# Optimization experiments

Measured on AMD Instinct MI355X. Metric: run time of the kernel, lower is better.

## Reference

```python
import jax, jax.numpy as jnp
import numpy as np

N_HEADS = 16
D_MODEL = 1024
D_K = D_MODEL // N_HEADS
B, T = 2, 2048


def setup_inputs() -> dict:
    key = jax.random.key(0)
    ks = jax.random.split(key, 12)
    s = 1.0 / np.sqrt(D_MODEL)
    inp = {
        "q": jax.random.normal(ks[0], (B, T, D_MODEL), jnp.float32),
        "k": jax.random.normal(ks[1], (B, T, D_MODEL), jnp.float32),
        "v": jax.random.normal(ks[2], (B, T, D_MODEL), jnp.float32),
        # weights stored as [in, out] (torch Linear weight transposed)
        "Wq": jax.random.normal(ks[3], (D_MODEL, D_MODEL), jnp.float32) * s,
        "bq": jax.random.normal(ks[4], (D_MODEL,), jnp.float32) * s,
        "Wk": jax.random.normal(ks[5], (D_MODEL, D_MODEL), jnp.float32) * s,
        "bk": jax.random.normal(ks[6], (D_MODEL,), jnp.float32) * s,
        "Wv": jax.random.normal(ks[7], (D_MODEL, D_MODEL), jnp.float32) * s,
        "bv": jax.random.normal(ks[8], (D_MODEL,), jnp.float32) * s,
        "Wo": jax.random.normal(ks[9], (D_MODEL, D_MODEL), jnp.float32) * s,
        "bo": jax.random.normal(ks[10], (D_MODEL,), jnp.float32) * s,
        "alpha": jnp.ones((1, N_HEADS, 1, 1), jnp.float32) * 10.0,
    }
    return inp


def reference(q, k, v, Wq, bq, Wk, bk, Wv, bv, Wo, bo, alpha):
    Bsz, Tlen, _ = q.shape

    def proj(x, W, b):
        # [B,T,D] -> [B,H,T,d_k]
        y = x @ W + b
        return y.reshape(Bsz, Tlen, N_HEADS, D_K).transpose(0, 2, 1, 3)

    qh = proj(q, Wq, bq)
    kh = proj(k, Wk, bk)
    vh = proj(v, Wv, bv)

    scores = jnp.einsum("bhqd,bhkd->bhqk", qh, kh)  # [B,H,T,T]
    norm_q = jnp.linalg.norm(qh, axis=-1)  # [B,H,T]
    norm_k = jnp.linalg.norm(kh, axis=-1)  # [B,H,T]
    D_udps = (norm_q[..., :, None] + norm_k[..., None, :]) ** 2  # [B,H,T,T]
    D_safe = jnp.where(D_udps == 0.0, jnp.inf, D_udps)
    scores = alpha * 4.0 * scores / D_safe
    attn = jax.nn.softmax(scores, axis=-1)
    out = jnp.einsum("bhqk,bhkd->bhqd", attn, vh)
    out = out.transpose(0, 2, 1, 3).reshape(Bsz, Tlen, D_MODEL)
    return out @ Wo + bo
```

## Files before the change

kernel.cpp:

```cpp
#include <hip/hip_runtime.h>
#include <hip/hip_bf16.h>

#define N_HEADS 16
#define D_MODEL 1024
#define D_K     64
#define B_SZ    2
#define T_LEN   2048
#define M_ROWS  (B_SZ * T_LEN)

typedef __bf16 bf16;
typedef __bf16 bf16x4 __attribute__((ext_vector_type(4)));
typedef __bf16 bf16x8 __attribute__((ext_vector_type(8)));
typedef float  f32x4  __attribute__((ext_vector_type(4)));
typedef unsigned int u32;

__device__ __forceinline__ void gload16(const bf16* g, bf16* l) {
    __builtin_amdgcn_global_load_lds(
        (const __attribute__((address_space(1))) u32*)g,
        (__attribute__((address_space(3))) u32*)l, 16, 0, 0);
}

#define WAIT_VM(N) asm volatile("s_waitcnt vmcnt(" #N ")" ::: "memory")

__global__ void wt_kernel(const float* __restrict__ W0, const float* __restrict__ W1,
                          const float* __restrict__ W2, const float* __restrict__ W3,
                          bf16* __restrict__ T0, bf16* __restrict__ T1,
                          bf16* __restrict__ T2, bf16* __restrict__ T3) {
    __shared__ float tile[32][33];
    const int z = blockIdx.z;
    const float* W = (z == 0) ? W0 : (z == 1) ? W1 : (z == 2) ? W2 : W3;
    bf16* Wt       = (z == 0) ? T0 : (z == 1) ? T1 : (z == 2) ? T2 : T3;
    const int tx = threadIdx.x, ty = threadIdx.y;
    const int x0 = blockIdx.x * 32, y0 = blockIdx.y * 32;
    for (int yy = ty; yy < 32; yy += 8)
        tile[yy][tx] = W[(size_t)(y0 + yy) * D_MODEL + x0 + tx];
    __syncthreads();
    for (int yy = ty; yy < 32; yy += 8)
        Wt[(size_t)(x0 + yy) * D_MODEL + y0 + tx] = (bf16)tile[tx][yy];
}

__global__ void conv3_kernel(const float* __restrict__ q, const float* __restrict__ k,
                             const float* __restrict__ v,
                             bf16* __restrict__ qb, bf16* __restrict__ kb,
                             bf16* __restrict__ vb) {
    const int z = blockIdx.y;
    const float* X = (z == 0) ? q : (z == 1) ? k : v;
    bf16* Y        = (z == 0) ? qb : (z == 1) ? kb : vb;
    const size_t i = ((size_t)blockIdx.x * 256 + threadIdx.x) * 8;
    const float4 v0 = *(const float4*)&X[i];
    const float4 v1 = *(const float4*)&X[i + 4];
    bf16x8 y;
    y[0]=(bf16)v0.x; y[1]=(bf16)v0.y; y[2]=(bf16)v0.z; y[3]=(bf16)v0.w;
    y[4]=(bf16)v1.x; y[5]=(bf16)v1.y; y[6]=(bf16)v1.z; y[7]=(bf16)v1.w;
    *(bf16x8*)&Y[i] = y;
}

__global__ __launch_bounds__(256, 3) void proj_kernel(
    const bf16* __restrict__ qb, const bf16* __restrict__ kb, const bf16* __restrict__ vb,
    const bf16* __restrict__ WtQ, const bf16* __restrict__ WtK, const bf16* __restrict__ WtV,
    const float* __restrict__ bqp, const float* __restrict__ bkp, const float* __restrict__ bvp,
    bf16* __restrict__ qh, bf16* __restrict__ kh, bf16* __restrict__ vt,
    float* __restrict__ nq, float* __restrict__ nk)
{
    __shared__ bf16 As[3][128 * 32];
    __shared__ bf16 Bs[3][128 * 32];

    const int hw      = blockIdx.x;
    const int logical = (hw & 7) * 96 + (hw >> 3);
    const int z       = logical >> 8;
    const int r       = logical & 255;
    const int m0      = (r >> 3) * 128;
    const int n0      = (r & 7) * 128;

    const bf16*  A    = (z == 0) ? qb  : (z == 1) ? kb  : vb;
    const bf16*  Bt   = (z == 0) ? WtQ : (z == 1) ? WtK : WtV;
    const float* bias = (z == 0) ? bqp : (z == 1) ? bkp : bvp;
    bf16* Out         = (z == 0) ? qh  : (z == 1) ? kh  : vt;

    const int tid = threadIdx.x, lane = tid & 63, w = tid >> 6;
    const int wm = w >> 1, wn = w & 1, g = lane >> 4, c = lane & 15;

    const int srow = w * 32 + (lane >> 2);
    const int scol = (lane & 3) * 8;
    const bf16* Ag = A  + (size_t)(m0 + srow) * D_MODEL + scol;
    const bf16* Bg = Bt + (size_t)(n0 + srow) * D_MODEL + scol;

    f32x4 acc[4][4] = {};

#define PSTAGE(buf, kk)                                                         \
    do {                                                                        \
        gload16(Ag + (kk),                  &As[buf][(w * 32) * 32]);           \
        gload16(Ag + 16 * D_MODEL + (kk),   &As[buf][(w * 32 + 16) * 32]);      \
        gload16(Bg + (kk),                  &Bs[buf][(w * 32) * 32]);           \
        gload16(Bg + 16 * D_MODEL + (kk),   &Bs[buf][(w * 32 + 16) * 32]);      \
    } while (0)

    PSTAGE(0, 0);
    PSTAGE(1, 32);
    WAIT_VM(4);
    __builtin_amdgcn_s_barrier();

    int cur = 0;
    for (int t = 0; t < 32; ++t) {
        if (t + 2 < 32) {
            int pre = cur + 2; if (pre >= 3) pre -= 3;
            PSTAGE(pre, (t + 2) * 32);
        }

        bf16x8 a[4], b[4];
        #pragma unroll
        for (int i = 0; i < 4; i++) a[i] = *(const bf16x8*)&As[cur][(wm*64 + i*16 + c) * 32 + g*8];
        #pragma unroll
        for (int j = 0; j < 4; j++) b[j] = *(const bf16x8*)&Bs[cur][(wn*64 + j*16 + c) * 32 + g*8];

        __builtin_amdgcn_s_setprio(1);
        if (z != 2) {
            #pragma unroll
            for (int i = 0; i < 4; i++)
                #pragma unroll
                for (int j = 0; j < 4; j++)
                    acc[i][j] = __builtin_amdgcn_mfma_f32_16x16x32_bf16(a[i], b[j], acc[i][j], 0, 0, 0);
        } else {
            #pragma unroll
            for (int i = 0; i < 4; i++)
                #pragma unroll
                for (int j = 0; j < 4; j++)
                    acc[i][j] = __builtin_amdgcn_mfma_f32_16x16x32_bf16(b[j], a[i], acc[i][j], 0, 0, 0);
        }
        __builtin_amdgcn_s_setprio(0);

        if (t + 2 < 32) { WAIT_VM(4); }
        else            { WAIT_VM(0); }
        __builtin_amdgcn_s_barrier();
        cur = (cur + 1 == 3) ? 0 : cur + 1;
    }
#undef PSTAGE

    if (z != 2) {
        float* nrm = (z == 0) ? nq : nk;
        const int h_ = (n0 >> 6) + wn;
        #pragma unroll
        for (int i = 0; i < 4; i++)
            #pragma unroll
            for (int r4 = 0; r4 < 4; r4++) {
                const int mrow = m0 + wm*64 + i*16 + g*4 + r4;
                const int b_ = mrow >> 11, t_ = mrow & (T_LEN - 1);
                float ss = 0.f;
                #pragma unroll
                for (int j = 0; j < 4; j++) {
                    const int ncol = n0 + wn*64 + j*16 + c;
                    const float y = acc[i][j][r4] + bias[ncol];
                    Out[(((size_t)(b_*N_HEADS + h_))*T_LEN + t_)*D_K + j*16 + c] = (bf16)y;
                    ss += y * y;
                }
                ss += __shfl_xor(ss, 1, 64);
                ss += __shfl_xor(ss, 2, 64);
                ss += __shfl_xor(ss, 4, 64);
                ss += __shfl_xor(ss, 8, 64);
                if (c == 0)
                    nrm[((size_t)(b_*N_HEADS + h_))*T_LEN + t_] = sqrtf(ss);
            }
    } else {
        #pragma unroll
        for (int i = 0; i < 4; i++)
            #pragma unroll
            for (int j = 0; j < 4; j++)
                #pragma unroll
                for (int r4 = 0; r4 < 4; r4++) {
                    const int nrow = n0 + wn*64 + j*16 + g*4 + r4;
                    const int mcol = m0 + wm*64 + i*16 + c;
                    const float y = acc[i][j][r4] + bias[nrow];
                    const int b_ = mcol >> 11, t_ = mcol & (T_LEN - 1);
                    const int h2 = nrow >> 6,  d_ = nrow & (D_K - 1);
                    Out[(((size_t)(b_*N_HEADS + h2))*D_K + d_)*T_LEN + t_] = (bf16)y;
                }
    }
}

#define KVB 64

__global__ __launch_bounds__(512, 4) void attn_kernel(
    const bf16* __restrict__ qh, const bf16* __restrict__ kh, const bf16* __restrict__ vt,
    const float* __restrict__ nq, const float* __restrict__ nk,
    const float* __restrict__ alpha, bf16* __restrict__ ao)
{
    __shared__ bf16 Ks[3][KVB * D_K];
    __shared__ bf16 Vs[3][KVB * D_K];
    __shared__ bf16 plds[8][16][72];

    const int bid     = blockIdx.x;
    const int logical = (bid & 7) * 64 + (bid >> 3);
    const int bh      = logical >> 4;
    const int q0b     = (logical & 15) * 128;

    const int tid  = threadIdx.x;
    const int w    = tid >> 6;
    const int lane = tid & 63;
    const int g    = lane >> 4, c = lane & 15;
    const int myq  = q0b + w * 16 + c;
    const int sw   = (c & 7) << 4;

    const int srow = tid >> 3;
    const int sgb  = (((tid & 7) ^ (srow & 7)) << 4);

    const bf16* Q  = qh + (size_t)bh * T_LEN * D_K;
    const bf16* K  = kh + (size_t)bh * T_LEN * D_K;
    const bf16* V  = vt + (size_t)bh * D_K * T_LEN;
    const float* NK = nk + (size_t)bh * T_LEN;

    const float al   = alpha[bh & (N_HEADS - 1)];
    const float a4   = al * 4.0f * 1.44269504f;
    const float negM = -(al * 1.44269504f) - 1e-4f;

    const bf16x8 bq0 = *(const bf16x8*)&Q[(size_t)myq * D_K + g*8];
    const bf16x8 bq1 = *(const bf16x8*)&Q[(size_t)myq * D_K + 32 + g*8];
    const float nq_own = nq[(size_t)bh * T_LEN + myq];

    bf16x8 ones;
    #pragma unroll
    for (int e = 0; e < 8; e++) ones[e] = (bf16)1.0f;

    f32x4 o[4] = {};
    f32x4 o4  = {};

#define AKSTAGE(buf, kn)                                                                          \
    do {                                                                                          \
        gload16((const bf16*)((const char*)&K[(size_t)((kn) + srow) * D_K] + sgb), &Ks[buf][w * 512]); \
        gload16((const bf16*)((const char*)&V[(size_t)srow * T_LEN + (kn)] + sgb), &Vs[buf][w * 512]); \
    } while (0)

#define SM(cb)                                                                  \
    do {                                                                        \
        const float nkr0 = nk4[cb].x, nkr1 = nk4[cb].y,                         \
                    nkr2 = nk4[cb].z, nkr3 = nk4[cb].w;                         \
        bf16x4 pk;                                                              \
        float den, rr, x;                                                       \
        den = nq_own + nkr0; rr = __builtin_amdgcn_rcpf(den);                   \
        x = __builtin_fmaf(a4 * S[cb][0], rr * rr, negM);                       \
        pk[0] = (bf16)__builtin_amdgcn_exp2f(x);                                \
        den = nq_own + nkr1; rr = __builtin_amdgcn_rcpf(den);                   \
        x = __builtin_fmaf(a4 * S[cb][1], rr * rr, negM);                       \
        pk[1] = (bf16)__builtin_amdgcn_exp2f(x);                                \
        den = nq_own + nkr2; rr = __builtin_amdgcn_rcpf(den);                   \
        x = __builtin_fmaf(a4 * S[cb][2], rr * rr, negM);                       \
        pk[2] = (bf16)__builtin_amdgcn_exp2f(x);                                \
        den = nq_own + nkr3; rr = __builtin_amdgcn_rcpf(den);                   \
        x = __builtin_fmaf(a4 * S[cb][3], rr * rr, negM);                       \
        pk[3] = (bf16)__builtin_amdgcn_exp2f(x);                                \
        *(bf16x4*)&plds[w][c][(cb)*16 + g*4] = pk;                              \
    } while (0)

#define PV(ks)                                                                  \
    do {                                                                        \
        const bf16x8 pb = *(const bf16x8*)&plds[w][c][(ks)*32 + g*8];           \
        __builtin_amdgcn_s_setprio(1);                                          \
        _Pragma("unroll")                                                       \
        for (int f = 0; f < 4; f++) {                                           \
            const char* vbase = (const char*)&Vs[cur][(size_t)(f*16 + c) * D_K];\
            const bf16x8 vb = *(const bf16x8*)(vbase + (((ks)*64 + g*16) ^ sw));\
            o[f] = __builtin_amdgcn_mfma_f32_16x16x32_bf16(vb, pb, o[f], 0, 0, 0);\
        }                                                                       \
        o4 = __builtin_amdgcn_mfma_f32_16x16x32_bf16(ones, pb, o4, 0, 0, 0);    \
        __builtin_amdgcn_s_setprio(0);                                          \
    } while (0)

    AKSTAGE(0, 0);
    AKSTAGE(1, KVB);
    WAIT_VM(2);
    __builtin_amdgcn_s_barrier();

    const int NT = T_LEN / KVB;
    int cur = 0;
    for (int t = 0; t < NT; ++t) {
        const int k0 = t * KVB;

        float4 nk4[4];
        #pragma unroll
        for (int cb = 0; cb < 4; cb++) nk4[cb] = *(const float4*)&NK[k0 + cb*16 + g*4];
        __builtin_amdgcn_sched_barrier(0);

        if (t + 2 < NT) {
            int pre = cur + 2; if (pre >= 3) pre -= 3;
            AKSTAGE(pre, k0 + 2*KVB);
        }

        f32x4 S[4];
        __builtin_amdgcn_s_setprio(1);
        #pragma unroll
        for (int cb = 0; cb < 4; cb++) {
            const char* kbase = (const char*)&Ks[cur][(size_t)(cb*16 + c) * D_K];
            const bf16x8 ka = *(const bf16x8*)(kbase + ((g*16) ^ sw));
            const bf16x8 kb = *(const bf16x8*)(kbase + ((64 + g*16) ^ sw));
            f32x4 s = {};
            s = __builtin_amdgcn_mfma_f32_16x16x32_bf16(ka, bq0, s, 0, 0, 0);
            s = __builtin_amdgcn_mfma_f32_16x16x32_bf16(kb, bq1, s, 0, 0, 0);
            S[cb] = s;
        }
        __builtin_amdgcn_s_setprio(0);

        SM(0); SM(1);
        PV(0);
        SM(2); SM(3);
        PV(1);

        if (t + 2 < NT) { WAIT_VM(2); }
        else            { WAIT_VM(0); }
        __builtin_amdgcn_s_barrier();
        cur = (cur + 1 == 3) ? 0 : cur + 1;
    }
#undef AKSTAGE
#undef SM
#undef PV

    const int b_ = bh >> 4, h_ = bh & 15;
    const float inv = 1.0f / o4[0];
    #pragma unroll
    for (int f = 0; f < 4; f++) {
        bf16x4 w4;
        #pragma unroll
        for (int r = 0; r < 4; r++) w4[r] = (bf16)(o[f][r] * inv);
        *(bf16x4*)&ao[((size_t)(b_*T_LEN + myq))*D_MODEL + h_*D_K + f*16 + g*4] = w4;
    }
}

__global__ __launch_bounds__(256, 4) void gemmo_kernel(
    const bf16* __restrict__ A, const bf16* __restrict__ Bt,
    const float* __restrict__ bias, float* __restrict__ Out)
{
    __shared__ bf16 As[2][64 * 32];
    __shared__ bf16 Bs[2][128 * 32];

    const int hw      = blockIdx.x;
    const int logical = (hw & 7) * 64 + (hw >> 3);
    const int m0      = (logical >> 3) * 64;
    const int n0      = (logical & 7) * 128;

    const int tid = threadIdx.x, lane = tid & 63, w = tid >> 6;
    const int wm = w >> 1, wn = w & 1, g = lane >> 4, c = lane & 15;

    const int arow = w * 16 + (lane >> 2);
    const int brow = w * 32 + (lane >> 2);
    const int scol = (lane & 3) * 8;
    const bf16* Ag = A  + (size_t)(m0 + arow) * D_MODEL + scol;
    const bf16* Bg = Bt + (size_t)(n0 + brow) * D_MODEL + scol;

    f32x4 acc[2][4] = {};

#define OSTAGE(buf, kk)                                                         \
    do {                                                                        \
        gload16(Ag + (kk),                &As[buf][(w * 16) * 32]);             \
        gload16(Bg + (kk),                &Bs[buf][(w * 32) * 32]);             \
        gload16(Bg + 16 * D_MODEL + (kk), &Bs[buf][(w * 32 + 16) * 32]);        \
    } while (0)

    OSTAGE(0, 0);
    __syncthreads();

    int cur = 0;
    for (int t = 0; t < 32; ++t) {
        if (t < 31) OSTAGE(cur ^ 1, (t + 1) * 32);

        bf16x8 a[2], b[4];
        #pragma unroll
        for (int i = 0; i < 2; i++) a[i] = *(const bf16x8*)&As[cur][(wm*32 + i*16 + c) * 32 + g*8];
        #pragma unroll
        for (int j = 0; j < 4; j++) b[j] = *(const bf16x8*)&Bs[cur][(wn*64 + j*16 + c) * 32 + g*8];

        __builtin_amdgcn_s_setprio(1);
        #pragma unroll
        for (int i = 0; i < 2; i++)
            #pragma unroll
            for (int j = 0; j < 4; j++)
                acc[i][j] = __builtin_amdgcn_mfma_f32_16x16x32_bf16(a[i], b[j], acc[i][j], 0, 0, 0);
        __builtin_amdgcn_s_setprio(0);
        __syncthreads();
        cur ^= 1;
    }
#undef OSTAGE

    #pragma unroll
    for (int i = 0; i < 2; i++)
        #pragma unroll
        for (int j = 0; j < 4; j++) {
            const int ncol = n0 + wn*64 + j*16 + c;
            const float bb = bias[ncol];
            #pragma unroll
            for (int r = 0; r < 4; r++) {
                const int mrow = m0 + wm*32 + i*16 + g*4 + r;
                Out[(size_t)mrow * D_MODEL + ncol] = acc[i][j][r] + bb;
            }
        }
}

extern "C" void kernel_launch(void* const* d_in, const int* in_sizes, int n_in,
                              void* d_out, int out_size, void* d_ws, size_t ws_size,
                              hipStream_t stream) {
    const float* q     = (const float*)d_in[0];
    const float* k     = (const float*)d_in[1];
    const float* v     = (const float*)d_in[2];
    const float* Wq    = (const float*)d_in[3];
    const float* bq    = (const float*)d_in[4];
    const float* Wk    = (const float*)d_in[5];
    const float* bk    = (const float*)d_in[6];
    const float* Wv    = (const float*)d_in[7];
    const float* bv    = (const float*)d_in[8];
    const float* Wo    = (const float*)d_in[9];
    const float* bo    = (const float*)d_in[10];
    const float* alpha = (const float*)d_in[11];

    char* ws = (char*)d_ws;
    const size_t WBYTES = (size_t)D_MODEL * D_MODEL * sizeof(bf16);
    const size_t HBYTES = (size_t)B_SZ * N_HEADS * T_LEN * D_K * sizeof(bf16);
    const size_t NBYTES = (size_t)B_SZ * N_HEADS * T_LEN * sizeof(float);
    bf16* WtQ = (bf16*)ws;  ws += WBYTES;
    bf16* WtK = (bf16*)ws;  ws += WBYTES;
    bf16* WtV = (bf16*)ws;  ws += WBYTES;
    bf16* WtO = (bf16*)ws;  ws += WBYTES;
    bf16* qh  = (bf16*)ws;  ws += HBYTES;
    bf16* kh  = (bf16*)ws;  ws += HBYTES;
    bf16* vt  = (bf16*)ws;  ws += HBYTES;
    float* nq = (float*)ws; ws += NBYTES;
    float* nk = (float*)ws; ws += NBYTES;
    bf16* ao  = (bf16*)ws;  ws += HBYTES;
    bf16* qb  = (bf16*)ws;  ws += HBYTES;
    bf16* kb  = (bf16*)ws;  ws += HBYTES;
    bf16* vb  = ao;

    wt_kernel<<<dim3(32, 32, 4), dim3(32, 8), 0, stream>>>(
        Wq, Wk, Wv, Wo, WtQ, WtK, WtV, WtO);

    conv3_kernel<<<dim3(M_ROWS * D_MODEL / 8 / 256, 3), 256, 0, stream>>>(
        q, k, v, qb, kb, vb);

    proj_kernel<<<768, 256, 0, stream>>>(
        qb, kb, vb, WtQ, WtK, WtV, bq, bk, bv, qh, kh, vt, nq, nk);

    attn_kernel<<<512, 512, 0, stream>>>(qh, kh, vt, nq, nk, alpha, ao);

    gemmo_kernel<<<512, 256, 0, stream>>>(ao, WtO, bo, (float*)d_out);
}
```

Before: 149.5 us.

## Hoist V fragment loads and softmax scale out of inner loop; triple-buffer output GEMM

In the attention kernel, all V fragments for a tile are loaded from LDS into registers up front, and the per-key scale a4/(nq+nk)^2 is computed once into a small register array, so the softmax and PV macros only do FMA, exp and MFMA. The output projection GEMM moves from double to triple buffering with explicit vmcnt waits and raw barriers, prefetching two K-steps ahead. The cost is higher register pressure from holding the V fragments and scales, plus 50% more LDS in the GEMM, which may reduce occupancy.

```diff
diff --git a/kernel.cpp b/kernel.cpp
--- a/kernel.cpp
+++ b/kernel.cpp
@@ -231,22 +231,15 @@
 
 #define SM(cb)                                                                  \
     do {                                                                        \
-        const float nkr0 = nk4[cb].x, nkr1 = nk4[cb].y,                         \
-                    nkr2 = nk4[cb].z, nkr3 = nk4[cb].w;                         \
         bf16x4 pk;                                                              \
-        float den, rr, x;                                                       \
-        den = nq_own + nkr0; rr = __builtin_amdgcn_rcpf(den);                   \
-        x = __builtin_fmaf(a4 * S[cb][0], rr * rr, negM);                       \
-        pk[0] = (bf16)__builtin_amdgcn_exp2f(x);                                \
-        den = nq_own + nkr1; rr = __builtin_amdgcn_rcpf(den);                   \
-        x = __builtin_fmaf(a4 * S[cb][1], rr * rr, negM);                       \
-        pk[1] = (bf16)__builtin_amdgcn_exp2f(x);                                \
-        den = nq_own + nkr2; rr = __builtin_amdgcn_rcpf(den);                   \
-        x = __builtin_fmaf(a4 * S[cb][2], rr * rr, negM);                       \
-        pk[2] = (bf16)__builtin_amdgcn_exp2f(x);                                \
-        den = nq_own + nkr3; rr = __builtin_amdgcn_rcpf(den);                   \
-        x = __builtin_fmaf(a4 * S[cb][3], rr * rr, negM);                       \
-        pk[3] = (bf16)__builtin_amdgcn_exp2f(x);                                \
+        pk[0] = (bf16)__builtin_amdgcn_exp2f(                                   \
+            __builtin_fmaf(S[cb][0], rd2[cb][0], negM));                        \
+        pk[1] = (bf16)__builtin_amdgcn_exp2f(                                   \
+            __builtin_fmaf(S[cb][1], rd2[cb][1], negM));                        \
+        pk[2] = (bf16)__builtin_amdgcn_exp2f(                                   \
+            __builtin_fmaf(S[cb][2], rd2[cb][2], negM));                        \
+        pk[3] = (bf16)__builtin_amdgcn_exp2f(                                   \
+            __builtin_fmaf(S[cb][3], rd2[cb][3], negM));                        \
         *(bf16x4*)&plds[w][c][(cb)*16 + g*4] = pk;                              \
     } while (0)
 
@@ -255,11 +248,8 @@
         const bf16x8 pb = *(const bf16x8*)&plds[w][c][(ks)*32 + g*8];           \
         __builtin_amdgcn_s_setprio(1);                                          \
         _Pragma("unroll")                                                       \
-        for (int f = 0; f < 4; f++) {                                           \
-            const char* vbase = (const char*)&Vs[cur][(size_t)(f*16 + c) * D_K];\
-            const bf16x8 vb = *(const bf16x8*)(vbase + (((ks)*64 + g*16) ^ sw));\
-            o[f] = __builtin_amdgcn_mfma_f32_16x16x32_bf16(vb, pb, o[f], 0, 0, 0);\
-        }                                                                       \
+        for (int f = 0; f < 4; f++)                                             \
+            o[f] = __builtin_amdgcn_mfma_f32_16x16x32_bf16(vbr[ks][f], pb, o[f], 0, 0, 0); \
         o4 = __builtin_amdgcn_mfma_f32_16x16x32_bf16(ones, pb, o4, 0, 0, 0);    \
         __builtin_amdgcn_s_setprio(0);                                          \
     } while (0)
@@ -298,6 +288,27 @@
         }
         __builtin_amdgcn_s_setprio(0);
 
+        bf16x8 vbr[2][4];
+        #pragma unroll
+        for (int ks = 0; ks < 2; ks++)
+            #pragma unroll
+            for (int f = 0; f < 4; f++) {
+                const char* vbase = (const char*)&Vs[cur][(size_t)(f*16 + c) * D_K];
+                vbr[ks][f] = *(const bf16x8*)(vbase + ((ks*64 + g*16) ^ sw));
+            }
+
+        float rd2[4][4];
+        #pragma unroll
+        for (int cb = 0; cb < 4; cb++) {
+            const float nkr[4] = {nk4[cb].x, nk4[cb].y, nk4[cb].z, nk4[cb].w};
+            #pragma unroll
+            for (int r = 0; r < 4; r++) {
+                const float den = nq_own + nkr[r];
+                const float rr  = __builtin_amdgcn_rcpf(den);
+                rd2[cb][r] = (a4 * rr) * rr;
+            }
+        }
+
         SM(0); SM(1);
         PV(0);
         SM(2); SM(3);
@@ -327,8 +338,8 @@
     const bf16* __restrict__ A, const bf16* __restrict__ Bt,
     const float* __restrict__ bias, float* __restrict__ Out)
 {
-    __shared__ bf16 As[2][64 * 32];
-    __shared__ bf16 Bs[2][128 * 32];
+    __shared__ bf16 As[3][64 * 32];
+    __shared__ bf16 Bs[3][128 * 32];
 
     const int hw      = blockIdx.x;
     const int logical = (hw & 7) * 64 + (hw >> 3);
@@ -354,11 +365,16 @@
     } while (0)
 
     OSTAGE(0, 0);
-    __syncthreads();
+    OSTAGE(1, 32);
+    WAIT_VM(3);
+    __builtin_amdgcn_s_barrier();
 
     int cur = 0;
     for (int t = 0; t < 32; ++t) {
-        if (t < 31) OSTAGE(cur ^ 1, (t + 1) * 32);
+        if (t + 2 < 32) {
+            int pre = cur + 2; if (pre >= 3) pre -= 3;
+            OSTAGE(pre, (t + 2) * 32);
+        }
 
         bf16x8 a[2], b[4];
         #pragma unroll
@@ -373,8 +389,11 @@
             for (int j = 0; j < 4; j++)
                 acc[i][j] = __builtin_amdgcn_mfma_f32_16x16x32_bf16(a[i], b[j], acc[i][j], 0, 0, 0);
         __builtin_amdgcn_s_setprio(0);
-        __syncthreads();
-        cur ^= 1;
+
+        if (t + 2 < 32) { WAIT_VM(3); }
+        else            { WAIT_VM(0); }
+        __builtin_amdgcn_s_barrier();
+        cur = (cur + 1 == 3) ? 0 : cur + 1;
     }
 #undef OSTAGE
 
```

New measurement: 149.7 us, median of 2. No clear change (+0.2%).
